# Optimization experiments

Measured on AMD Instinct MI355X. Metric: run time of the kernel, lower is better.

Reference implementation:

```python
import jax, jax.numpy as jnp
import numpy as np


def _lstm_scan(x, W, U, b):
    """Unidirectional Keras-style LSTM over x: [B, T, F] -> [B, T, H].
    Gate order (i, f, c, o); sigmoid recurrent activation, tanh activation."""
    B = x.shape[0]
    H = U.shape[0]
    # Precompute input projections for all timesteps: [B, T, 4H]
    xp = jnp.einsum('btf,fg->btg', x, W) + b

    def step(carry, xt):
        h, c = carry
        z = xt + h @ U  # [B, 4H]
        i, f, g, o = jnp.split(z, 4, axis=-1)
        i = jax.nn.sigmoid(i)
        f = jax.nn.sigmoid(f)
        g = jnp.tanh(g)
        o = jax.nn.sigmoid(o)
        c = f * c + i * g
        h = o * jnp.tanh(c)
        return (h, c), h

    init = (jnp.zeros((B, H), x.dtype), jnp.zeros((B, H), x.dtype))
    _, hs = jax.lax.scan(step, init, xp.transpose(1, 0, 2))  # [T, B, H]
    return hs.transpose(1, 0, 2)


def _bidir(x, Wf, Uf, bf, Wb, Ub, bb):
    fwd = _lstm_scan(x, Wf, Uf, bf)
    bwd = jnp.flip(_lstm_scan(jnp.flip(x, axis=1), Wb, Ub, bb), axis=1)
    return jnp.concatenate([fwd, bwd], axis=-1)  # merge_mode='concat'


def setup_inputs() -> dict:
    key = jax.random.key(0)
    ks = jax.random.split(key, 16)
    B, T, F, H = 64, 1024, 64, 256
    s_in0 = 1.0 / np.sqrt(F)
    s_in1 = 1.0 / np.sqrt(2 * H)
    s_rec = 1.0 / np.sqrt(H)
    inp = {
        'x': jax.random.normal(ks[0], (B, T, F), jnp.float32),
        'W0f': jax.random.normal(ks[1], (F, 4 * H), jnp.float32) * s_in0,
        'U0f': jax.random.normal(ks[2], (H, 4 * H), jnp.float32) * s_rec,
        'b0f': jnp.zeros((4 * H,), jnp.float32),
        'W0b': jax.random.normal(ks[3], (F, 4 * H), jnp.float32) * s_in0,
        'U0b': jax.random.normal(ks[4], (H, 4 * H), jnp.float32) * s_rec,
        'b0b': jnp.zeros((4 * H,), jnp.float32),
        'W1f': jax.random.normal(ks[5], (2 * H, 4 * H), jnp.float32) * s_in1,
        'U1f': jax.random.normal(ks[6], (H, 4 * H), jnp.float32) * s_rec,
        'b1f': jnp.zeros((4 * H,), jnp.float32),
        'W1b': jax.random.normal(ks[7], (2 * H, 4 * H), jnp.float32) * s_in1,
        'U1b': jax.random.normal(ks[8], (H, 4 * H), jnp.float32) * s_rec,
        'b1b': jnp.zeros((4 * H,), jnp.float32),
        'Wd': jax.random.normal(ks[9], (2 * H, 1), jnp.float32) * s_in1,
        'bd': jnp.zeros((1,), jnp.float32),
    }
    return inp


def reference(x, W0f, U0f, b0f, W0b, U0b, b0b,
              W1f, U1f, b1f, W1b, U1b, b1b, Wd, bd):
    # Layer 0 bidirectional LSTM -> [B, T, 2H]; dropout is identity at inference
    h = _bidir(x, W0f, U0f, b0f, W0b, U0b, b0b)
    # Layer 1 bidirectional LSTM -> [B, T, 2H]
    h = _bidir(h, W1f, U1f, b1f, W1b, U1b, b1b)
    # Dense(1, linear) head -> [B, T, 1]
    return jnp.einsum('btd,do->bto', h, Wd) + bd
```

## Files before the change

kernel.cpp:

```cpp
#include <hip/hip_runtime.h>
#include <hip/hip_bf16.h>
#include <cstdint>
#include <cstddef>

#define B_ 64
#define T_ 1024

typedef _Float16 half_t;
typedef __attribute__((ext_vector_type(8))) _Float16 half8;
typedef __attribute__((ext_vector_type(4))) float f32x4;
typedef __attribute__((ext_vector_type(8))) unsigned short ushort8;

__device__ __forceinline__ float sigm(float x) { return 1.f / (1.f + __expf(-x)); }
__device__ __forceinline__ float tanh_fast(float x) {
  float e = __expf(2.f * x);
  return 1.f - 2.f / (e + 1.f);
}

__global__ __launch_bounds__(256) void permute_cols(const float* __restrict__ src,
                                                    float* __restrict__ dst, int K) {
  int idx = blockIdx.x * 256 + threadIdx.x;
  if (idx >= K * 1024) return;
  int n = idx & 1023;
  size_t k = (size_t)(idx >> 10);
  dst[idx] = src[(k << 10) + ((size_t)(n & 3) << 8) + (n >> 2)];
}

__global__ __launch_bounds__(256) void pack_u_mfma(const float* __restrict__ src,
                                                   half_t* __restrict__ dst) {
  int tid = blockIdx.x * 256 + threadIdx.x;
  int l = tid & 63;
  int s = (tid >> 6) & 7;
  int n = (tid >> 9) & 1;
  int w = (tid >> 10) & 3;
  int wgc = (tid >> 12) & 7;
  int col = wgc * 128 + w * 32 + n * 16 + (l & 15);
  int hc = col >> 2, g = col & 3;
  int k0 = s * 32 + (l >> 4) * 8;
  half8 v;
#pragma unroll
  for (int j = 0; j < 8; ++j)
    v[j] = (half_t)src[(size_t)(k0 + j) * 1024 + (g << 8) + hc];
  *(half8*)(dst + (size_t)tid * 8) = v;
}

__global__ __launch_bounds__(256) void pack_w0_mfma(const float* __restrict__ src,
                                                    half_t* __restrict__ dst) {
  int line = blockIdx.x * 256 + threadIdx.x;
  int l = line & 63;
  int ks = (line >> 6) & 1;
  int n = (line >> 7) & 1;
  int w = (line >> 8) & 3;
  int wgc = (line >> 10) & 7;
  int col = wgc * 128 + w * 32 + n * 16 + (l & 15);
  int sc = ((col & 3) << 8) + (col >> 2);
  int k0 = ks * 32 + (l >> 4) * 8;
  half8 v;
#pragma unroll
  for (int j = 0; j < 8; ++j)
    v[j] = (half_t)src[(size_t)(k0 + j) * 1024 + sc];
  *(half8*)(dst + (size_t)line * 8) = v;
}

__global__ __launch_bounds__(256) void pack_w1_mfma(const float* __restrict__ src,
                                                    half_t* __restrict__ dst) {
  int tid = blockIdx.x * 256 + threadIdx.x;
  int l = tid & 63;
  int ks = (tid >> 6) & 15;
  int nb = tid >> 10;
  int colp = nb * 16 + (l & 15);
  int sc = ((colp & 3) << 8) + (colp >> 2);
  int k0 = ks * 32 + (l >> 4) * 8;
  half8 v;
#pragma unroll
  for (int j = 0; j < 8; ++j)
    v[j] = (half_t)src[(size_t)(k0 + j) * 1024 + sc];
  *(half8*)(dst + (size_t)tid * 8) = v;
}

__global__ __launch_bounds__(256) void pack_x_f16(const float* __restrict__ x,
                                                  unsigned short* __restrict__ xi) {
  int idx = blockIdx.x * 256 + threadIdx.x;
  int b = idx & 15;
  int q = (idx >> 4) & 3;
  int ks = (idx >> 6) & 1;
  int t = (idx >> 7) & 1023;
  int bg = idx >> 17;
  const float* src = x + ((size_t)(bg * 16 + b) * T_ + t) * 64 + ks * 32 + q * 8;
  ushort8 v;
#pragma unroll
  for (int j = 0; j < 8; ++j) {
    half_t h = (half_t)src[j];
    v[j] = __builtin_bit_cast(unsigned short, h);
  }
  *(ushort8*)(xi + (size_t)idx * 8) = v;
}

__global__ __launch_bounds__(256) void init_out(float* __restrict__ out,
                                                const float* __restrict__ bd, int n) {
  int i = blockIdx.x * 256 + threadIdx.x;
  if (i < n) out[i] = bd[0];
}

__global__ __launch_bounds__(256) void diag_out(float* __restrict__ out, int n, float v) {
  int i = blockIdx.x * 256 + threadIdx.x;
  if (i < n) out[i] = (i == 0) ? v : 0.f;
}

__global__ __launch_bounds__(256) void proj1_mfma(
    const unsigned short* __restrict__ h0,
    const half_t* __restrict__ Wf, const half_t* __restrict__ Wb,
    const float* __restrict__ bpf, const float* __restrict__ bpb,
    float* __restrict__ xp, int s0, int Tc) {
  const int dir = blockIdx.z;
  const half_t* Wpk = dir ? Wb : Wf;
  const float* bs = dir ? bpb : bpf;
  const int b = blockIdx.y;
  const int mt = blockIdx.x;
  const int tid = threadIdx.x;
  const int l = tid & 63, w = tid >> 6;

  __shared__ __align__(16) unsigned short A_lds[16][520];

  {
    int r = tid >> 4, c16 = tid & 15;
    int sl = mt * 16 + r;
    int t = dir ? (T_ - 1 - s0 - sl) : (s0 + sl);
    const ushort8* srcp =
        (const ushort8*)(h0 + ((size_t)b * T_ + t) * 512 + c16 * 32);
#pragma unroll
    for (int u = 0; u < 4; ++u)
      *(ushort8*)&A_lds[r][c16 * 32 + u * 8] = __builtin_nontemporal_load(srcp + u);
  }
  __syncthreads();

  f32x4 acc[16];
#pragma unroll
  for (int n = 0; n < 16; ++n) acc[n] = (f32x4){0.f, 0.f, 0.f, 0.f};

  for (int ks = 0; ks < 16; ++ks) {
    half8 a = *(const half8*)&A_lds[l & 15][ks * 32 + (l >> 4) * 8];
    const half_t* bp_ = Wpk + (((size_t)(w * 16) * 16 + ks) * 64 + l) * 8;
#pragma unroll
    for (int n = 0; n < 16; ++n) {
      half8 bfr = *(const half8*)(bp_ + (size_t)n * 16 * 64 * 8);
      acc[n] = __builtin_amdgcn_mfma_f32_16x16x32_f16(a, bfr, acc[n], 0, 0, 0);
    }
  }

#pragma unroll
  for (int n = 0; n < 16; ++n) {
    int col = (w * 16 + n) * 16 + (l & 15);
    float bias = bs[col];
#pragma unroll
    for (int r = 0; r < 4; ++r) {
      int sl = mt * 16 + (l >> 4) * 4 + r;
      __builtin_nontemporal_store(
          acc[n][r] + bias,
          &xp[(((size_t)dir * B_ + b) * Tc + sl) * 1024 + col]);
    }
  }
}

template <int L0>
__global__ __launch_bounds__(512, 1) void lstm_scan_mfma(
    const float* __restrict__ xp,
    const unsigned short* __restrict__ xi,
    const half_t* __restrict__ W0f_, const half_t* __restrict__ W0b_,
    const float* __restrict__ b0f_, const float* __restrict__ b0b_,
    const half_t* __restrict__ Upk_f, const half_t* __restrict__ Upk_b,
    float* __restrict__ carry_c,
    unsigned* __restrict__ payl, unsigned* __restrict__ flagw,
    int s0, int Tc, int tagbase,
    unsigned short* __restrict__ hout,
    const float* __restrict__ Wd, float* __restrict__ out,
    const unsigned short* __restrict__ h0src,
    const half_t* __restrict__ W1f_, const half_t* __restrict__ W1b_,
    const float* __restrict__ bp1f_, const float* __restrict__ bp1b_,
    float* __restrict__ xpn, int s0p) {
  __shared__ __align__(16) unsigned short shmem[16 * 520];
  const int tid = threadIdx.x;

  if (!L0 && blockIdx.x >= 32) {
    unsigned short(*A2)[520] = (unsigned short(*)[520])shmem;
    int pb = blockIdx.x - 32;
    int mpt = Tc / 16;
    int mt = pb % mpt;
    int b = (pb / mpt) % B_;
    int dir = pb / (mpt * B_);
    const half_t* Wpk = dir ? W1b_ : W1f_;
    const float* bs = dir ? bp1b_ : bp1f_;
    const int l = tid & 63, w = tid >> 6;

    if (tid < 256) {
      int r = tid >> 4, c16 = tid & 15;
      int sl = mt * 16 + r;
      int t = dir ? (T_ - 1 - s0p - sl) : (s0p + sl);
      const ushort8* srcp =
          (const ushort8*)(h0src + ((size_t)b * T_ + t) * 512 + c16 * 32);
#pragma unroll
      for (int u = 0; u < 4; ++u)
        *(ushort8*)&A2[r][c16 * 32 + u * 8] = __builtin_nontemporal_load(srcp + u);
    }
    __syncthreads();
    if (tid < 256) {
      f32x4 acc[16];
#pragma unroll
      for (int n = 0; n < 16; ++n) acc[n] = (f32x4){0.f, 0.f, 0.f, 0.f};
      for (int ks = 0; ks < 16; ++ks) {
        half8 a = *(const half8*)&A2[l & 15][ks * 32 + (l >> 4) * 8];
        const half_t* bp_ = Wpk + (((size_t)(w * 16) * 16 + ks) * 64 + l) * 8;
#pragma unroll
        for (int n = 0; n < 16; ++n) {
          half8 bfr = *(const half8*)(bp_ + (size_t)n * 16 * 64 * 8);
          acc[n] = __builtin_amdgcn_mfma_f32_16x16x32_f16(a, bfr, acc[n], 0, 0, 0);
        }
      }
#pragma unroll
      for (int n = 0; n < 16; ++n) {
        int col = (w * 16 + n) * 16 + (l & 15);
        float bias = bs[col];
#pragma unroll
        for (int r = 0; r < 4; ++r) {
          int sl = mt * 16 + (l >> 4) * 4 + r;
          __builtin_nontemporal_store(
              acc[n][r] + bias,
              &xpn[(((size_t)dir * B_ + b) * Tc + sl) * 1024 + col]);
        }
      }
    }
    return;
  }

  unsigned short* A_lds = shmem;
  unsigned short* hstage = shmem + 4096;
  float* red_sm = (float*)(shmem + 5120);

  const int blk = blockIdx.x;
  const int unit = blk & 7;
  const int wgc = blk >> 3;
  const int dir = unit & 1;
  const int bg = unit >> 1;
  const int b0u = bg * 16;
  const int l = tid & 63;
  const int w8 = tid >> 6;
  const int wgco = wgc * 2 + (w8 >> 2);
  const int w = w8 & 3;

  const half_t* Upk = dir ? Upk_b : Upk_f;
  half8 U[2][8];
  {
    const half_t* up = Upk + (size_t)(wgco * 4 + w) * 8192;
#pragma unroll
    for (int n = 0; n < 2; ++n)
#pragma unroll
      for (int s = 0; s < 8; ++s)
        U[n][s] = *(const half8*)(up + ((size_t)(n * 8 + s) * 64 + l) * 8);
  }

  const int b_lane = 4 * (l >> 4) + (l & 3);
  const int hcb = wgco * 32 + w * 8 + ((l >> 2) & 3);
  const int colb = wgco * 128 + w * 32 + (l & 15);
  float cst[2];
#pragma unroll
  for (int n = 0; n < 2; ++n)
    cst[n] = (s0 == 0) ? 0.f
        : carry_c[((size_t)dir * B_ + b0u + b_lane) * 256 + hcb + n * 4];

  float wdl[2] = {0.f, 0.f};
  half8 W0r[2][2];
  float bias0[2] = {0.f, 0.f};
  const unsigned short* xib = nullptr;
  if (L0) {
    const half_t* W0pk = dir ? W0b_ : W0f_;
    const float* bs0 = dir ? b0b_ : b0f_;
#pragma unroll
    for (int n = 0; n < 2; ++n) {
      bias0[n] = bs0[colb + n * 16];
#pragma unroll
      for (int ks = 0; ks < 2; ++ks)
        W0r[n][ks] = *(const half8*)(W0pk +
            ((size_t)(((wgco * 4 + w) * 2 + n) * 2 + ks) * 64 + l) * 8);
    }
    xib = xi + (size_t)bg * T_ * 1024;
  } else {
    wdl[0] = Wd[dir * 256 + hcb];
    wdl[1] = Wd[dir * 256 + hcb + 4];
  }

  unsigned* payl_u = payl + (size_t)unit * 4096;
  unsigned* flag_u = flagw + unit * 16;

  if (s0 == 0) {
#pragma unroll
    for (int i = 0; i < 4; ++i) ((unsigned*)A_lds)[tid * 4 + i] = 0u;
  } else {
    unsigned dd[4];
#pragma unroll
    for (int i = 0; i < 4; ++i)
      dd[i] = __hip_atomic_load(payl_u + 2048 + tid * 4 + i,
                                __ATOMIC_RELAXED, __HIP_MEMORY_SCOPE_AGENT);
#pragma unroll
    for (int i = 0; i < 4; ++i)
      ((unsigned*)A_lds)[tid * 4 + i] = dd[i];
  }
  __syncthreads();

  const float* xpu = L0 ? nullptr : (xp + (size_t)(dir * B_ + b0u) * Tc * 1024);

  float xpre[2][4];
  half8 xfre[2];
  {
    if (L0) {
      int t0f = dir ? (T_ - 1 - s0) : s0;
#pragma unroll
      for (int ks = 0; ks < 2; ++ks)
        xfre[ks] = __builtin_nontemporal_load(
            (const half8*)((const half_t*)xib + (size_t)t0f * 1024 +
                           ((ks * 4 + (l >> 4)) * 16 + (l & 15)) * 8));
    } else {
#pragma unroll
      for (int n = 0; n < 2; ++n)
#pragma unroll
        for (int r = 0; r < 4; ++r)
          xpre[n][r] = __builtin_nontemporal_load(
              &xpu[((size_t)(4 * (l >> 4) + r) * Tc) * 1024 + colb + n * 16]);
    }
  }

  const int hbl = (w8 >> 2) * 512 + (w * 16 + b_lane) * 8 + ((l >> 2) & 3);

  for (int sl = 0; sl < Tc; ++sl) {
    const int s = s0 + sl;
    const int t = dir ? (T_ - 1 - s) : s;
    const int slot = s & 1;

    f32x4 acc[2];
    if (L0) {
#pragma unroll
      for (int n = 0; n < 2; ++n)
#pragma unroll
        for (int r = 0; r < 4; ++r) acc[n][r] = bias0[n];
      half8 xa0 = xfre[0], xa1 = xfre[1];
#pragma unroll
      for (int n = 0; n < 2; ++n) {
        acc[n] = __builtin_amdgcn_mfma_f32_16x16x32_f16(xa0, W0r[n][0], acc[n], 0, 0, 0);
        acc[n] = __builtin_amdgcn_mfma_f32_16x16x32_f16(xa1, W0r[n][1], acc[n], 0, 0, 0);
      }
    } else {
#pragma unroll
      for (int n = 0; n < 2; ++n)
#pragma unroll
        for (int r = 0; r < 4; ++r) acc[n][r] = xpre[n][r];
    }

    half8 a[8];
#pragma unroll
    for (int sK = 0; sK < 8; ++sK)
      a[sK] = *(const half8*)&((const half_t*)A_lds)[((sK * 4 + (l >> 4)) * 16 + (l & 15)) * 8];

#pragma unroll
    for (int sK = 0; sK < 8; ++sK) {
      acc[0] = __builtin_amdgcn_mfma_f32_16x16x32_f16(a[sK], U[0][sK], acc[0], 0, 0, 0);
      acc[1] = __builtin_amdgcn_mfma_f32_16x16x32_f16(a[sK], U[1][sK], acc[1], 0, 0, 0);
    }

    float vhead = 0.f;
    unsigned short hu2[2];
#pragma unroll
    for (int n = 0; n < 2; ++n) {
      float v0 = acc[n][0], v1 = acc[n][1], v2 = acc[n][2], v3 = acc[n][3];
      float x0 = __shfl_xor(v1, 1), x1 = __shfl_xor(v0, 1);
      float x2 = __shfl_xor(v3, 1), x3 = __shfl_xor(v2, 1);
      float a0 = (l & 1) ? x0 : v0;
      float a1 = (l & 1) ? v1 : x1;
      float a2 = (l & 1) ? x2 : v2;
      float a3 = (l & 1) ? v3 : x3;
      float y0 = __shfl_xor(a2, 2), y1 = __shfl_xor(a3, 2);
      float y2 = __shfl_xor(a0, 2), y3 = __shfl_xor(a1, 2);
      float u0 = (l & 2) ? y0 : a0;
      float u1 = (l & 2) ? y1 : a1;
      float u2 = (l & 2) ? a2 : y2;
      float u3 = (l & 2) ? a3 : y3;

      float iG = sigm(u0), fG = sigm(u1), gG = tanh_fast(u2), oG = sigm(u3);
      float cn = fG * cst[n] + iG * gG;
      cst[n] = cn;
      float h = oG * tanh_fast(cn);

      if (!L0) vhead += h * wdl[n];
      hu2[n] = __builtin_bit_cast(unsigned short, (half_t)h);
      if (sl == Tc - 1)
        carry_c[((size_t)dir * B_ + b0u + b_lane) * 256 + hcb + n * 4] = cn;
    }
    hstage[hbl] = hu2[0];
    hstage[hbl + 4] = hu2[1];
    if (!L0) {
      vhead += __shfl_xor(vhead, 4);
      vhead += __shfl_xor(vhead, 8);
      if ((l & 12) == 0) red_sm[w8 * 16 + b_lane] = vhead;
    }
    __syncthreads();

    const unsigned* hs32 = (const unsigned*)hstage;
    __hip_atomic_store(payl_u + slot * 2048 + wgc * 512 + tid, hs32[tid],
                       __ATOMIC_RELAXED, __HIP_MEMORY_SCOPE_AGENT);

    asm volatile("s_waitcnt vmcnt(0)" ::: "memory");
    __syncthreads();
    const unsigned want = (unsigned)(tagbase + s + 1);
    if (tid == 0)
      __hip_atomic_store(flag_u + slot * 8 + wgc, want,
                         __ATOMIC_RELAXED, __HIP_MEMORY_SCOPE_AGENT);

    if (L0) {
      int sub = tid >> 8, r = tid & 255;
      int bb = r >> 4, cc = r & 15;
      __builtin_nontemporal_store(
          hs32[sub * 256 + (cc >> 2) * 64 + bb * 4 + (cc & 3)],
          (unsigned*)hout + ((size_t)(b0u + bb) * T_ + t) * 256 + dir * 128 +
              (wgc * 2 + sub) * 16 + cc);
    } else if (tid < 16) {
      float sum = ((red_sm[tid] + red_sm[16 + tid]) +
                   (red_sm[32 + tid] + red_sm[48 + tid])) +
                  ((red_sm[64 + tid] + red_sm[80 + tid]) +
                   (red_sm[96 + tid] + red_sm[112 + tid]));
      atomicAdd(out + (((size_t)(b0u + tid)) << 10) + t, sum);
    }

    if (sl + 1 < Tc) {
      if (L0) {
        int tn = dir ? (T_ - 2 - s) : (s + 1);
#pragma unroll
        for (int ks = 0; ks < 2; ++ks)
          xfre[ks] = __builtin_nontemporal_load(
              (const half8*)((const half_t*)xib + (size_t)tn * 1024 +
                             ((ks * 4 + (l >> 4)) * 16 + (l & 15)) * 8));
      } else {
#pragma unroll
        for (int n = 0; n < 2; ++n)
#pragma unroll
          for (int r = 0; r < 4; ++r)
            xpre[n][r] = __builtin_nontemporal_load(
                &xpu[((size_t)(4 * (l >> 4) + r) * Tc + sl + 1) * 1024 + colb + n * 16]);
      }

      if (tid < 4 && tid != wgc) {
        while (__hip_atomic_load(flag_u + slot * 8 + tid, __ATOMIC_RELAXED,
                                 __HIP_MEMORY_SCOPE_AGENT) != want) {}
      }
      __syncthreads();
      unsigned dd[4];
      const int g = tid >> 6;
      if ((g >> 1) == wgc) {
#pragma unroll
        for (int i = 0; i < 4; ++i)
          dd[i] = hs32[(g & 1) * 256 + (tid & 63) * 4 + i];
      } else {
#pragma unroll
        for (int i = 0; i < 4; ++i)
          dd[i] = __hip_atomic_load(payl_u + slot * 2048 + tid * 4 + i,
                                    __ATOMIC_RELAXED, __HIP_MEMORY_SCOPE_AGENT);
      }
#pragma unroll
      for (int i = 0; i < 4; ++i)
        ((unsigned*)A_lds)[tid * 4 + i] = dd[i];
      __syncthreads();
    }
  }
}

extern "C" void kernel_launch(void* const* d_in, const int* in_sizes, int n_in,
                              void* d_out, int out_size, void* d_ws, size_t ws_size,
                              hipStream_t stream) {
  const float* x   = (const float*)d_in[0];
  const float* W0f = (const float*)d_in[1];
  const float* U0f = (const float*)d_in[2];
  const float* b0f = (const float*)d_in[3];
  const float* W0b = (const float*)d_in[4];
  const float* U0b = (const float*)d_in[5];
  const float* b0b = (const float*)d_in[6];
  const float* W1f = (const float*)d_in[7];
  const float* U1f = (const float*)d_in[8];
  const float* b1f = (const float*)d_in[9];
  const float* W1b = (const float*)d_in[10];
  const float* U1b = (const float*)d_in[11];
  const float* b1b = (const float*)d_in[12];
  const float* Wd  = (const float*)d_in[13];
  const float* bd  = (const float*)d_in[14];
  float* out = (float*)d_out;
  char* ws = (char*)d_ws;

  const size_t H0_BYTES   = (size_t)B_ * T_ * 512 * 2;
  const size_t UPK_BYTES  = (size_t)262144 * 2;
  const size_t W0PK_BYTES = (size_t)8192 * 8 * 2;
  const size_t W1PK_BYTES = (size_t)512 * 1024 * 2;
  const size_t XI_BYTES   = (size_t)B_ * T_ * 64 * 2;
  const size_t BP_BYTES   = 1024 * 4;
  const size_t CC_BYTES   = (size_t)2 * B_ * 256 * 4;
  const size_t PL_BYTES   = (size_t)8 * 4096 * 4;
  const size_t FL_BYTES   = 1024;
  const size_t REPACK = 4 * UPK_BYTES + 2 * W0PK_BYTES + 2 * W1PK_BYTES +
                        XI_BYTES + 4 * BP_BYTES + CC_BYTES + PL_BYTES +
                        FL_BYTES + 1024;

  int Tc = 0;
  for (int tc = 128; tc >= 64; tc >>= 1) {
    size_t xpb = (size_t)2 * B_ * tc * 1024 * 4;
    if (H0_BYTES + REPACK + 2 * xpb <= ws_size) { Tc = tc; break; }
  }
  if (!Tc) {
    float v = 1000.f + (float)(ws_size >> 20);
    diag_out<<<(out_size + 255) / 256, 256, 0, stream>>>(out, out_size, v);
    return;
  }
  const size_t XP_BYTES = (size_t)2 * B_ * Tc * 1024 * 4;

  size_t off = 0;
  unsigned short* h0 = (unsigned short*)(ws + off); off += H0_BYTES;
  half_t* Up00 = (half_t*)(ws + off); off += UPK_BYTES;
  half_t* Up01 = (half_t*)(ws + off); off += UPK_BYTES;
  half_t* Up10 = (half_t*)(ws + off); off += UPK_BYTES;
  half_t* Up11 = (half_t*)(ws + off); off += UPK_BYTES;
  half_t* W0pf = (half_t*)(ws + off); off += W0PK_BYTES;
  half_t* W0pb = (half_t*)(ws + off); off += W0PK_BYTES;
  half_t* W1pf = (half_t*)(ws + off); off += W1PK_BYTES;
  half_t* W1pb = (half_t*)(ws + off); off += W1PK_BYTES;
  unsigned short* xi = (unsigned short*)(ws + off); off += XI_BYTES;
  float* bp0f = (float*)(ws + off); off += BP_BYTES;
  float* bp0b = (float*)(ws + off); off += BP_BYTES;
  float* bp1f = (float*)(ws + off); off += BP_BYTES;
  float* bp1b = (float*)(ws + off); off += BP_BYTES;
  float* carry_c = (float*)(ws + off); off += CC_BYTES;
  unsigned* payl = (unsigned*)(ws + off); off += PL_BYTES;
  unsigned* flagw = (unsigned*)(ws + off); off += FL_BYTES;
  off = (off + 255) & ~(size_t)255;
  float* xpA = (float*)(ws + off); off += XP_BYTES;
  float* xpB = (float*)(ws + off);

  pack_u_mfma<<<128, 256, 0, stream>>>(U0f, Up00);
  pack_u_mfma<<<128, 256, 0, stream>>>(U0b, Up01);
  pack_u_mfma<<<128, 256, 0, stream>>>(U1f, Up10);
  pack_u_mfma<<<128, 256, 0, stream>>>(U1b, Up11);
  pack_w0_mfma<<<32, 256, 0, stream>>>(W0f, W0pf);
  pack_w0_mfma<<<32, 256, 0, stream>>>(W0b, W0pb);
  pack_w1_mfma<<<256, 256, 0, stream>>>(W1f, W1pf);
  pack_w1_mfma<<<256, 256, 0, stream>>>(W1b, W1pb);
  pack_x_f16<<<2048, 256, 0, stream>>>(x, xi);
  permute_cols<<<4, 256, 0, stream>>>(b0f, bp0f, 1);
  permute_cols<<<4, 256, 0, stream>>>(b0b, bp0b, 1);
  permute_cols<<<4, 256, 0, stream>>>(b1f, bp1f, 1);
  permute_cols<<<4, 256, 0, stream>>>(b1b, bp1b, 1);

  lstm_scan_mfma<1><<<32, 512, 0, stream>>>(
      nullptr, xi, W0pf, W0pb, bp0f, bp0b, Up00, Up01, carry_c,
      payl, flagw, 0, T_, 0, h0, nullptr, nullptr,
      nullptr, nullptr, nullptr, nullptr, nullptr, nullptr, 0);

  init_out<<<(out_size + 255) / 256, 256, 0, stream>>>(out, bd, out_size);
  const int nch = T_ / Tc;
  const int nproj = (Tc / 16) * B_ * 2;
  proj1_mfma<<<dim3(Tc / 16, B_, 2), 256, 0, stream>>>(
      h0, W1pf, W1pb, bp1f, bp1b, xpA, 0, Tc);
  for (int ci = 0; ci < nch; ++ci) {
    int s0c = ci * Tc;
    float* xcur = (ci & 1) ? xpB : xpA;
    float* xnext = (ci & 1) ? xpA : xpB;
    int extra = (ci + 1 < nch) ? nproj : 0;
    lstm_scan_mfma<0><<<32 + extra, 512, 0, stream>>>(
        xcur, nullptr, nullptr, nullptr, nullptr, nullptr, Up10, Up11, carry_c,
        payl, flagw, s0c, Tc, 1024, nullptr, Wd, out,
        h0, W1pf, W1pb, bp1f, bp1b, xnext, (ci + 1) * Tc);
  }
}
```

Before: 5.928 ms.

## Run each LSTM scan unit on two 1024-thread blocks instead of four

The recurrent scan is repartitioned so each (direction, batch-group) unit uses two 1024-thread workgroups instead of four 512-thread ones. Each step now waits on a single peer flag rather than three, and more of the hidden state is exchanged through LDS instead of global memory. The interleaved next-chunk projection blocks are also widened to 1024 threads, with each wave computing four output tiles. In exchange the kernel gets a bigger per-block barrier and a longer 16-wave reduction, and runs on fewer CUs with more waves per CU.

```diff
diff --git a/kernel.cpp b/kernel.cpp
--- a/kernel.cpp
+++ b/kernel.cpp
@@ -163,7 +163,7 @@
 }
 
 template <int L0>
-__global__ __launch_bounds__(512, 1) void lstm_scan_mfma(
+__global__ __launch_bounds__(1024, 1) void lstm_scan_mfma(
     const float* __restrict__ xp,
     const unsigned short* __restrict__ xi,
     const half_t* __restrict__ W0f_, const half_t* __restrict__ W0b_,
@@ -181,52 +181,47 @@
   __shared__ __align__(16) unsigned short shmem[16 * 520];
   const int tid = threadIdx.x;
 
-  if (!L0 && blockIdx.x >= 32) {
+  if (!L0 && blockIdx.x >= 16) {
     unsigned short(*A2)[520] = (unsigned short(*)[520])shmem;
-    int pb = blockIdx.x - 32;
+    int pb = blockIdx.x - 16;
     int mpt = Tc / 16;
     int mt = pb % mpt;
     int b = (pb / mpt) % B_;
     int dir = pb / (mpt * B_);
     const half_t* Wpk = dir ? W1b_ : W1f_;
     const float* bs = dir ? bp1b_ : bp1f_;
-    const int l = tid & 63, w = tid >> 6;
-
-    if (tid < 256) {
-      int r = tid >> 4, c16 = tid & 15;
+    const int l = tid & 63, w16 = tid >> 6;
+
+    {
+      int r = tid >> 6, c8 = tid & 63;
       int sl = mt * 16 + r;
       int t = dir ? (T_ - 1 - s0p - sl) : (s0p + sl);
-      const ushort8* srcp =
-          (const ushort8*)(h0src + ((size_t)b * T_ + t) * 512 + c16 * 32);
-#pragma unroll
-      for (int u = 0; u < 4; ++u)
-        *(ushort8*)&A2[r][c16 * 32 + u * 8] = __builtin_nontemporal_load(srcp + u);
+      *(ushort8*)&A2[r][c8 * 8] = __builtin_nontemporal_load(
+          (const ushort8*)(h0src + ((size_t)b * T_ + t) * 512 + c8 * 8));
     }
     __syncthreads();
-    if (tid < 256) {
-      f32x4 acc[16];
-#pragma unroll
-      for (int n = 0; n < 16; ++n) acc[n] = (f32x4){0.f, 0.f, 0.f, 0.f};
-      for (int ks = 0; ks < 16; ++ks) {
-        half8 a = *(const half8*)&A2[l & 15][ks * 32 + (l >> 4) * 8];
-        const half_t* bp_ = Wpk + (((size_t)(w * 16) * 16 + ks) * 64 + l) * 8;
-#pragma unroll
-        for (int n = 0; n < 16; ++n) {
-          half8 bfr = *(const half8*)(bp_ + (size_t)n * 16 * 64 * 8);
-          acc[n] = __builtin_amdgcn_mfma_f32_16x16x32_f16(a, bfr, acc[n], 0, 0, 0);
-        }
+    f32x4 acc[4];
+#pragma unroll
+    for (int n = 0; n < 4; ++n) acc[n] = (f32x4){0.f, 0.f, 0.f, 0.f};
+    for (int ks = 0; ks < 16; ++ks) {
+      half8 a = *(const half8*)&A2[l & 15][ks * 32 + (l >> 4) * 8];
+#pragma unroll
+      for (int n = 0; n < 4; ++n) {
+        int nb = w16 * 4 + n;
+        half8 bfr = *(const half8*)(Wpk + (((size_t)(nb * 16 + ks)) * 64 + l) * 8);
+        acc[n] = __builtin_amdgcn_mfma_f32_16x16x32_f16(a, bfr, acc[n], 0, 0, 0);
       }
-#pragma unroll
-      for (int n = 0; n < 16; ++n) {
-        int col = (w * 16 + n) * 16 + (l & 15);
-        float bias = bs[col];
-#pragma unroll
-        for (int r = 0; r < 4; ++r) {
-          int sl = mt * 16 + (l >> 4) * 4 + r;
-          __builtin_nontemporal_store(
-              acc[n][r] + bias,
-              &xpn[(((size_t)dir * B_ + b) * Tc + sl) * 1024 + col]);
-        }
+    }
+#pragma unroll
+    for (int n = 0; n < 4; ++n) {
+      int col = (w16 * 4 + n) * 16 + (l & 15);
+      float bias = bs[col];
+#pragma unroll
+      for (int r = 0; r < 4; ++r) {
+        int sl = mt * 16 + (l >> 4) * 4 + r;
+        __builtin_nontemporal_store(
+            acc[n][r] + bias,
+            &xpn[(((size_t)dir * B_ + b) * Tc + sl) * 1024 + col]);
       }
     }
     return;
@@ -234,18 +229,18 @@
 
   unsigned short* A_lds = shmem;
   unsigned short* hstage = shmem + 4096;
-  float* red_sm = (float*)(shmem + 5120);
+  float* red_sm = (float*)(shmem + 6144);
 
   const int blk = blockIdx.x;
   const int unit = blk & 7;
-  const int wgc = blk >> 3;
+  const int half = blk >> 3;
   const int dir = unit & 1;
   const int bg = unit >> 1;
   const int b0u = bg * 16;
   const int l = tid & 63;
-  const int w8 = tid >> 6;
-  const int wgco = wgc * 2 + (w8 >> 2);
-  const int w = w8 & 3;
+  const int w16 = tid >> 6;
+  const int wgco = half * 4 + (w16 >> 2);
+  const int w = w16 & 3;
 
   const half_t* Upk = dir ? Upk_b : Upk_f;
   half8 U[2][8];
@@ -292,17 +287,17 @@
   unsigned* flag_u = flagw + unit * 16;
 
   if (s0 == 0) {
-#pragma unroll
-    for (int i = 0; i < 4; ++i) ((unsigned*)A_lds)[tid * 4 + i] = 0u;
+    ((unsigned*)A_lds)[tid * 2] = 0u;
+    ((unsigned*)A_lds)[tid * 2 + 1] = 0u;
   } else {
-    unsigned dd[4];
-#pragma unroll
-    for (int i = 0; i < 4; ++i)
-      dd[i] = __hip_atomic_load(payl_u + 2048 + tid * 4 + i,
+    unsigned dd[2];
+#pragma unroll
+    for (int i = 0; i < 2; ++i)
+      dd[i] = __hip_atomic_load(payl_u + 2048 + tid * 2 + i,
                                 __ATOMIC_RELAXED, __HIP_MEMORY_SCOPE_AGENT);
 #pragma unroll
-    for (int i = 0; i < 4; ++i)
-      ((unsigned*)A_lds)[tid * 4 + i] = dd[i];
+    for (int i = 0; i < 2; ++i)
+      ((unsigned*)A_lds)[tid * 2 + i] = dd[i];
   }
   __syncthreads();
 
@@ -328,7 +323,7 @@
     }
   }
 
-  const int hbl = (w8 >> 2) * 512 + (w * 16 + b_lane) * 8 + ((l >> 2) & 3);
+  const int hbl = (w16 >> 2) * 512 + (w * 16 + b_lane) * 8 + ((l >> 2) & 3);
 
   for (int sl = 0; sl < Tc; ++sl) {
     const int s = s0 + sl;
@@ -398,19 +393,19 @@
     if (!L0) {
       vhead += __shfl_xor(vhead, 4);
       vhead += __shfl_xor(vhead, 8);
-      if ((l & 12) == 0) red_sm[w8 * 16 + b_lane] = vhead;
+      if ((l & 12) == 0) red_sm[w16 * 16 + b_lane] = vhead;
     }
     __syncthreads();
 
     const unsigned* hs32 = (const unsigned*)hstage;
-    __hip_atomic_store(payl_u + slot * 2048 + wgc * 512 + tid, hs32[tid],
+    __hip_atomic_store(payl_u + slot * 2048 + half * 1024 + tid, hs32[tid],
                        __ATOMIC_RELAXED, __HIP_MEMORY_SCOPE_AGENT);
 
     asm volatile("s_waitcnt vmcnt(0)" ::: "memory");
     __syncthreads();
     const unsigned want = (unsigned)(tagbase + s + 1);
     if (tid == 0)
-      __hip_atomic_store(flag_u + slot * 8 + wgc, want,
+      __hip_atomic_store(flag_u + slot * 8 + half, want,
                          __ATOMIC_RELAXED, __HIP_MEMORY_SCOPE_AGENT);
 
     if (L0) {
@@ -419,12 +414,11 @@
       __builtin_nontemporal_store(
           hs32[sub * 256 + (cc >> 2) * 64 + bb * 4 + (cc & 3)],
           (unsigned*)hout + ((size_t)(b0u + bb) * T_ + t) * 256 + dir * 128 +
-              (wgc * 2 + sub) * 16 + cc);
+              (half * 4 + sub) * 16 + cc);
     } else if (tid < 16) {
-      float sum = ((red_sm[tid] + red_sm[16 + tid]) +
-                   (red_sm[32 + tid] + red_sm[48 + tid])) +
-                  ((red_sm[64 + tid] + red_sm[80 + tid]) +
-                   (red_sm[96 + tid] + red_sm[112 + tid]));
+      float sum = 0.f;
+#pragma unroll
+      for (int ww = 0; ww < 16; ++ww) sum += red_sm[ww * 16 + tid];
       atomicAdd(out + (((size_t)(b0u + tid)) << 10) + t, sum);
     }
 
@@ -445,26 +439,25 @@
                 &xpu[((size_t)(4 * (l >> 4) + r) * Tc + sl + 1) * 1024 + colb + n * 16]);
       }
 
-      if (tid < 4 && tid != wgc) {
-        while (__hip_atomic_load(flag_u + slot * 8 + tid, __ATOMIC_RELAXED,
+      if (tid == 0) {
+        while (__hip_atomic_load(flag_u + slot * 8 + (half ^ 1),
+                                 __ATOMIC_RELAXED,
                                  __HIP_MEMORY_SCOPE_AGENT) != want) {}
       }
       __syncthreads();
-      unsigned dd[4];
-      const int g = tid >> 6;
-      if ((g >> 1) == wgc) {
-#pragma unroll
-        for (int i = 0; i < 4; ++i)
-          dd[i] = hs32[(g & 1) * 256 + (tid & 63) * 4 + i];
+      unsigned dd[2];
+      if ((tid >> 9) == half) {
+#pragma unroll
+        for (int i = 0; i < 2; ++i) dd[i] = hs32[tid * 2 - half * 1024 + i];
       } else {
 #pragma unroll
-        for (int i = 0; i < 4; ++i)
-          dd[i] = __hip_atomic_load(payl_u + slot * 2048 + tid * 4 + i,
+        for (int i = 0; i < 2; ++i)
+          dd[i] = __hip_atomic_load(payl_u + slot * 2048 + tid * 2 + i,
                                     __ATOMIC_RELAXED, __HIP_MEMORY_SCOPE_AGENT);
       }
 #pragma unroll
-      for (int i = 0; i < 4; ++i)
-        ((unsigned*)A_lds)[tid * 4 + i] = dd[i];
+      for (int i = 0; i < 2; ++i)
+        ((unsigned*)A_lds)[tid * 2 + i] = dd[i];
       __syncthreads();
     }
   }
@@ -552,7 +545,7 @@
   permute_cols<<<4, 256, 0, stream>>>(b1f, bp1f, 1);
   permute_cols<<<4, 256, 0, stream>>>(b1b, bp1b, 1);
 
-  lstm_scan_mfma<1><<<32, 512, 0, stream>>>(
+  lstm_scan_mfma<1><<<16, 1024, 0, stream>>>(
       nullptr, xi, W0pf, W0pb, bp0f, bp0b, Up00, Up01, carry_c,
       payl, flagw, 0, T_, 0, h0, nullptr, nullptr,
       nullptr, nullptr, nullptr, nullptr, nullptr, nullptr, 0);
@@ -567,7 +560,7 @@
     float* xcur = (ci & 1) ? xpB : xpA;
     float* xnext = (ci & 1) ? xpA : xpB;
     int extra = (ci + 1 < nch) ? nproj : 0;
-    lstm_scan_mfma<0><<<32 + extra, 512, 0, stream>>>(
+    lstm_scan_mfma<0><<<16 + extra, 1024, 0, stream>>>(
         xcur, nullptr, nullptr, nullptr, nullptr, nullptr, Up10, Up11, carry_c,
         payl, flagw, s0c, Tc, 1024, nullptr, Wd, out,
         h0, W1pf, W1pb, bp1f, bp1b, xnext, (ci + 1) * Tc);
```

Measured after the change: 9.541 ms. 60.9% more time.
